# Kernel optimization log

Hardware: AMD Instinct MI355X
Metric: run time of the kernel (lower is better)

Reference implementation:

```python
import jax, jax.numpy as jnp
import numpy as np

D = 2048
H = 16
HD = D // H
FF = 4 * D
EPS = 1e-5


def layernorm(x, scale, shift):
    mean = jnp.mean(x, axis=-1, keepdims=True)
    var = jnp.mean((x - mean) ** 2, axis=-1, keepdims=True)  # unbiased=False
    return scale * (x - mean) / jnp.sqrt(var + EPS) + shift


def setup_inputs() -> dict:
    key = jax.random.key(0)
    ks = jax.random.split(key, 12)
    s = 0.02
    return {
        "x": jax.random.normal(ks[0], (2, 2048, D), dtype=jnp.float32),
        "ln1_scale": jnp.ones((D,), jnp.float32),
        "ln1_shift": jnp.zeros((D,), jnp.float32),
        "wq": jax.random.normal(ks[1], (D, D), jnp.float32) * s,
        "bq": jnp.zeros((D,), jnp.float32),
        "wk": jax.random.normal(ks[2], (D, D), jnp.float32) * s,
        "bk": jnp.zeros((D,), jnp.float32),
        "wv": jax.random.normal(ks[3], (D, D), jnp.float32) * s,
        "bv": jnp.zeros((D,), jnp.float32),
        "wo": jax.random.normal(ks[4], (D, D), jnp.float32) * s,
        "bo": jnp.zeros((D,), jnp.float32),
        "ln2_scale": jnp.ones((D,), jnp.float32),
        "ln2_shift": jnp.zeros((D,), jnp.float32),
        "w1": jax.random.normal(ks[5], (D, FF), jnp.float32) * s,
        "b1": jnp.zeros((FF,), jnp.float32),
        "w2": jax.random.normal(ks[6], (FF, D), jnp.float32) * s,
        "b2": jnp.zeros((D,), jnp.float32),
    }


def block(x, ln1_scale, ln1_shift, wq, bq, wk, bk, wv, bv, wo, bo,
          ln2_scale, ln2_shift, w1, b1, w2, b2):
    B, S, _ = x.shape
    h = layernorm(x, ln1_scale, ln1_shift)
    q = (h @ wq + bq).reshape(B, S, H, HD).transpose(0, 2, 1, 3)  # [B,H,S,hd]
    k = (h @ wk + bk).reshape(B, S, H, HD).transpose(0, 2, 1, 3)
    v = (h @ wv + bv).reshape(B, S, H, HD).transpose(0, 2, 1, 3)
    scores = jnp.einsum("bhqd,bhkd->bhqk", q, k) / jnp.sqrt(jnp.float32(HD))
    causal = jnp.tril(jnp.ones((S, S), dtype=bool))
    scores = jnp.where(causal[None, None], scores, -jnp.inf)
    attn = jax.nn.softmax(scores, axis=-1)
    ctx = jnp.einsum("bhqk,bhkd->bhqd", attn, v)
    ctx = ctx.transpose(0, 2, 1, 3).reshape(B, S, D)
    x = x + (ctx @ wo + bo)
    h2 = layernorm(x, ln2_scale, ln2_shift)
    ffn = jax.nn.gelu(h2 @ w1 + b1, approximate=False) @ w2 + b2
    return x + ffn


def reference(x, ln1_scale, ln1_shift, wq, bq, wk, bk, wv, bv, wo, bo,
              ln2_scale, ln2_shift, w1, b1, w2, b2):
    return block(x, ln1_scale, ln1_shift, wq, bq, wk, bk, wv, bv, wo, bo,
                 ln2_scale, ln2_shift, w1, b1, w2, b2)
```

## Files before the change

### kernel.cpp

```cpp
#include <hip/hip_runtime.h>
#include <hip/hip_bf16.h>
#include <math.h>

namespace {

constexpr int Dm  = 2048;
constexpr int FFm = 8192;
constexpr int SEQ = 2048;
constexpr int HDm = 128;
constexpr int MR  = 4096;
constexpr int QW  = 3 * Dm;

typedef __bf16 bf16_t;
typedef __bf16 bf16x8 __attribute__((ext_vector_type(8)));
typedef float  f32x4  __attribute__((ext_vector_type(4)));

typedef __attribute__((address_space(1))) const void as1_void;
typedef __attribute__((address_space(3))) void as3_void;

__device__ __forceinline__ void gload_lds16(const void* g, void* l) {
  __builtin_amdgcn_global_load_lds((as1_void*)g, (as3_void*)l, 16, 0, 0);
}

__global__ __launch_bounds__(256)
void ln_kernel(const float* __restrict__ x, const float* __restrict__ sc,
               const float* __restrict__ sh, bf16_t* __restrict__ out)
{
  const int row = blockIdx.x;
  const int tid = threadIdx.x;
  const float4* xr = (const float4*)(x + (size_t)row * Dm);
  float4 v0 = xr[tid*2], v1 = xr[tid*2+1];
  float s  = v0.x+v0.y+v0.z+v0.w + v1.x+v1.y+v1.z+v1.w;
  float s2 = v0.x*v0.x+v0.y*v0.y+v0.z*v0.z+v0.w*v0.w
           + v1.x*v1.x+v1.y*v1.y+v1.z*v1.z+v1.w*v1.w;
  #pragma unroll
  for (int off = 32; off; off >>= 1) { s += __shfl_xor(s, off); s2 += __shfl_xor(s2, off); }
  __shared__ float red[8];
  if ((tid & 63) == 0) { red[(tid>>6)*2] = s; red[(tid>>6)*2+1] = s2; }
  __syncthreads();
  s  = red[0]+red[2]+red[4]+red[6];
  s2 = red[1]+red[3]+red[5]+red[7];
  const float mean = s * (1.f/Dm);
  const float var  = fmaxf(s2 * (1.f/Dm) - mean*mean, 0.f);
  const float rstd = rsqrtf(var + 1e-5f);
  const float4* scp = (const float4*)sc;
  const float4* shp = (const float4*)sh;
  float4 sc0 = scp[tid*2], sc1 = scp[tid*2+1];
  float4 sh0 = shp[tid*2], sh1 = shp[tid*2+1];
  __attribute__((aligned(16))) bf16_t ob[8];
  ob[0] = (bf16_t)((v0.x-mean)*rstd*sc0.x + sh0.x);
  ob[1] = (bf16_t)((v0.y-mean)*rstd*sc0.y + sh0.y);
  ob[2] = (bf16_t)((v0.z-mean)*rstd*sc0.z + sh0.z);
  ob[3] = (bf16_t)((v0.w-mean)*rstd*sc0.w + sh0.w);
  ob[4] = (bf16_t)((v1.x-mean)*rstd*sc1.x + sh1.x);
  ob[5] = (bf16_t)((v1.y-mean)*rstd*sc1.y + sh1.y);
  ob[6] = (bf16_t)((v1.z-mean)*rstd*sc1.z + sh1.z);
  ob[7] = (bf16_t)((v1.w-mean)*rstd*sc1.w + sh1.w);
  *(uint4*)(out + (size_t)row*Dm + tid*8) = *(const uint4*)ob;
}

__global__ __launch_bounds__(256)
void wconv4(const float* __restrict__ wq, const float* __restrict__ wk,
            const float* __restrict__ wv, const float* __restrict__ wo,
            bf16_t* __restrict__ dst)
{
  const int z = blockIdx.z;
  const float* W = (z == 0) ? wq : (z == 1) ? wk : (z == 2) ? wv : wo;
  bf16_t* WT = dst + (size_t)z * Dm * Dm;
  __shared__ float tile[32][33];
  const int tx = threadIdx.x & 31, ty = threadIdx.x >> 5;
  const int nb = blockIdx.x * 32, kb = blockIdx.y * 32;
  #pragma unroll
  for (int p = 0; p < 4; ++p)
    tile[ty+8*p][tx] = W[(size_t)(kb+ty+8*p)*Dm + nb + tx];
  __syncthreads();
  #pragma unroll
  for (int p = 0; p < 4; ++p)
    WT[(size_t)(nb+ty+8*p)*Dm + kb + tx] = (bf16_t)tile[tx][ty+8*p];
}

__global__ __launch_bounds__(256)
void wconv_t(const float* __restrict__ W, bf16_t* __restrict__ WT, int K, int N)
{
  __shared__ float tile[32][33];
  const int tx = threadIdx.x & 31, ty = threadIdx.x >> 5;
  const int nb = blockIdx.x * 32, kb = blockIdx.y * 32;
  #pragma unroll
  for (int p = 0; p < 4; ++p)
    tile[ty+8*p][tx] = W[(size_t)(kb+ty+8*p)*N + nb + tx];
  __syncthreads();
  #pragma unroll
  for (int p = 0; p < 4; ++p)
    WT[(size_t)(nb+ty+8*p)*K + kb + tx] = (bf16_t)tile[tx][ty+8*p];
}

__global__ void bias_concat(const float* __restrict__ bq, const float* __restrict__ bk,
                            const float* __restrict__ bv, float* __restrict__ o)
{
  int i = blockIdx.x*256 + threadIdx.x;
  o[i] = bq[i]; o[Dm+i] = bk[i]; o[2*Dm+i] = bv[i];
}

__global__ __launch_bounds__(256)
void vtrans(const bf16_t* __restrict__ qkv, bf16_t* __restrict__ vT)
{
  __shared__ bf16_t tile[32][33];
  const int tx = threadIdx.x & 31, ty = threadIdx.x >> 5;
  const int s0 = blockIdx.x*32, d0 = blockIdx.y*32, bh = blockIdx.z;
  const int b = bh >> 4, h = bh & 15;
  const bf16_t* src = qkv + (size_t)(b*SEQ)*QW + 2*Dm + h*HDm;
  #pragma unroll
  for (int p = 0; p < 4; ++p)
    tile[ty+8*p][tx] = src[(size_t)(s0+ty+8*p)*QW + d0 + tx];
  __syncthreads();
  bf16_t* dst = vT + (size_t)bh*HDm*SEQ;
  #pragma unroll
  for (int p = 0; p < 4; ++p)
    dst[(size_t)(d0+ty+8*p)*SEQ + s0 + tx] = tile[tx][ty+8*p];
}

template<int MODE>
__global__ __launch_bounds__(512, 2)
void gemm8p(const bf16_t* __restrict__ A, const bf16_t* __restrict__ BT,
            const float* __restrict__ bias,
            void* __restrict__ Cout, void* __restrict__ Cout2,
            int Ndim, int Kslice, int Kstride, int gn)
{
  const int gm = (int)gridDim.x / gn;
  const int cm = gm >> 1, cn = gn >> 2;
  const int c = blockIdx.x & 7;
  const int idx = blockIdx.x >> 3;
  const int mi = idx / cn, ni = idx - mi*cn;
  const int m0 = ((c >> 2)*cm + mi) * 256;
  const int n0 = ((c & 3)*cn + ni) * 256;
  const int kOff = blockIdx.y * Kslice;
  const int tid = threadIdx.x;
  const int lane = tid & 63;
  const int w = tid >> 6;
  const int wr = w >> 2, wc = w & 3;
  const int lr = lane & 15, kg = lane >> 4;

  __shared__ __attribute__((aligned(16))) bf16_t lds[65536];

  f32x4 acc[8][4] = {};

  const int r1   = tid >> 3;
  const int blk1 = (tid & 7) ^ (r1 & 7);
  const size_t rowoff = (size_t)64 * Kstride;
  const bf16_t* pA0 = A  + (size_t)(m0 + r1)*Kstride       + kOff + blk1*8;
  const bf16_t* pA1 = A  + (size_t)(m0 + 128 + r1)*Kstride + kOff + blk1*8;
  const bf16_t* pB0 = BT + (size_t)(n0 + r1)*Kstride       + kOff + blk1*8;
  const bf16_t* pB1 = BT + (size_t)(n0 + 128 + r1)*Kstride + kOff + blk1*8;
  bf16_t* const d0 = lds + (size_t)tid*8;

#define STG(p, region) do { \
    gload_lds16((p), d0 + (region)*8192); \
    gload_lds16((p) + rowoff, d0 + (region)*8192 + 4096); \
    (p) += 64; } while (0)

  auto readA = [&](int buf, int mh, bf16x8* f) {
    const bf16_t* base = lds + (buf*4 + wr)*8192;
    #pragma unroll
    for (int ml = 0; ml < 4; ++ml)
      #pragma unroll
      for (int kk = 0; kk < 2; ++kk) {
        const int row = mh*64 + ml*16 + lr;
        f[ml*2+kk] = *(const bf16x8*)(base + row*64 + (((kk*4+kg) ^ (row&7))*8));
      }
  };
  auto readB = [&](int buf, int nh, bf16x8* f) {
    const bf16_t* base = lds + (buf*4 + 2 + (wc>>1))*8192;
    #pragma unroll
    for (int nl = 0; nl < 2; ++nl)
      #pragma unroll
      for (int kk = 0; kk < 2; ++kk) {
        const int row = (wc&1)*64 + nh*32 + nl*16 + lr;
        f[nl*2+kk] = *(const bf16x8*)(base + row*64 + (((kk*4+kg) ^ (row&7))*8));
      }
  };
  auto mfma16 = [&](int mh, int nh, const bf16x8* Af, const bf16x8* Bf) {
    __builtin_amdgcn_s_setprio(1);
    #pragma unroll
    for (int ml = 0; ml < 4; ++ml)
      #pragma unroll
      for (int nl = 0; nl < 2; ++nl)
        #pragma unroll
        for (int kk = 0; kk < 2; ++kk)
          acc[mh*4+ml][nh*2+nl] =
            __builtin_amdgcn_mfma_f32_16x16x32_bf16(Af[ml*2+kk], Bf[nl*2+kk],
                                                    acc[mh*4+ml][nh*2+nl], 0, 0, 0);
    __builtin_amdgcn_s_setprio(0);
  };

#define PHASE_MID() do { __builtin_amdgcn_s_barrier(); \
    asm volatile("s_waitcnt lgkmcnt(0)"); } while (0)
#define PHASE_END() __builtin_amdgcn_s_barrier()
#define KGUARD(more_) do { if (more_) asm volatile("s_waitcnt vmcnt(4)" ::: "memory"); \
    else asm volatile("s_waitcnt vmcnt(0)" ::: "memory"); \
    __builtin_amdgcn_s_barrier(); } while (0)

  STG(pA0, 0); STG(pA1, 1); STG(pB0, 2); STG(pB1, 3);
  STG(pA0, 4); STG(pA1, 5);
  asm volatile("s_waitcnt vmcnt(4)" ::: "memory");
  __builtin_amdgcn_s_barrier();

  const int NITER = Kslice >> 7;
  for (int j = 0; j < NITER; ++j) {
    const bool more = (j + 1 < NITER);
    bf16x8 Af0[8], Af1[8], Bf0[4], Bf1[4];

    readA(0,0,Af0); readB(0,0,Bf0);
    STG(pB0, 6);
    PHASE_MID(); mfma16(0,0,Af0,Bf0); PHASE_END();
    readA(0,1,Af1);
    STG(pB1, 7);
    PHASE_MID(); mfma16(1,0,Af1,Bf0); PHASE_END();
    readB(0,1,Bf1);
    if (more) STG(pA0, 0);
    PHASE_MID(); mfma16(1,1,Af1,Bf1); PHASE_END();
    if (more) STG(pA1, 1);
    PHASE_MID(); mfma16(0,1,Af0,Bf1);
    KGUARD(more);

    readA(1,0,Af0); readB(1,0,Bf0);
    if (more) STG(pB0, 2);
    PHASE_MID(); mfma16(0,0,Af0,Bf0); PHASE_END();
    readA(1,1,Af1);
    if (more) STG(pB1, 3);
    PHASE_MID(); mfma16(1,0,Af1,Bf0); PHASE_END();
    readB(1,1,Bf1);
    if (more) STG(pA0, 4);
    PHASE_MID(); mfma16(1,1,Af1,Bf1); PHASE_END();
    if (more) STG(pA1, 5);
    PHASE_MID(); mfma16(0,1,Af0,Bf1);
    KGUARD(more);
  }
#undef PHASE_MID
#undef PHASE_END
#undef KGUARD
#undef STG

  const int cr0 = m0 + wr*128 + kg*4;
  float* pout = nullptr;
  if constexpr (MODE == 3) pout = (float*)(blockIdx.y ? Cout2 : Cout);
  #pragma unroll
  for (int nf = 0; nf < 4; ++nf) {
    const int col = n0 + wc*64 + nf*16 + lr;
    float bv = 0.f;
    if constexpr (MODE != 3) bv = bias[col];
    #pragma unroll
    for (int mf = 0; mf < 8; ++mf) {
      const int rbase = cr0 + mf*16;
      #pragma unroll
      for (int jj = 0; jj < 4; ++jj) {
        float v = acc[mf][nf][jj] + bv;
        const size_t idx = (size_t)(rbase + jj)*Ndim + col;
        if constexpr (MODE == 1) v = 0.5f*v*(1.f + erff(v*0.70710678118f));
        if constexpr (MODE == 0 || MODE == 1) ((bf16_t*)Cout)[idx] = (bf16_t)v;
        else pout[idx] = v;
      }
    }
  }
}

__global__ __launch_bounds__(256)
void splitk_reduce(const float* __restrict__ p0, const float* __restrict__ p1,
                   const float* __restrict__ bias, const float* __restrict__ resid,
                   float* __restrict__ out, int Ndim)
{
  const size_t e = ((size_t)blockIdx.x*256 + threadIdx.x) * 4;
  float4 a = *(const float4*)(p0 + e);
  float4 b = *(const float4*)(p1 + e);
  float4 r = *(const float4*)(resid + e);
  float4 bv = *(const float4*)(bias + (int)(e & (size_t)(Ndim - 1)));
  float4 o;
  o.x = a.x + b.x + bv.x + r.x;
  o.y = a.y + b.y + bv.y + r.y;
  o.z = a.z + b.z + bv.z + r.z;
  o.w = a.w + b.w + bv.w + r.w;
  *(float4*)(out + e) = o;
}

__global__ __launch_bounds__(512, 2)
void flash_attn3(const bf16_t* __restrict__ qkv, const bf16_t* __restrict__ vT,
                 bf16_t* __restrict__ ctx)
{
  const int bid = blockIdx.x;
  const int bh  = (bid & 7) + 8 * ((bid >> 3) & 3);
  const int qi  = 7 - (bid >> 5);
  const int b = bh >> 4, h = bh & 15;
  const int Q0 = qi * 256;
  const int tid = threadIdx.x;
  const int lane = tid & 63;
  const int w = tid >> 6;
  const int lr = lane & 15, kg = lane >> 4;
  const int q0w = Q0 + w * 32;

  __shared__ __attribute__((aligned(16))) bf16_t Ks[64*128];
  __shared__ __attribute__((aligned(16))) bf16_t Vs[128*64];
  __shared__ __attribute__((aligned(16))) bf16_t Plds[8*2048];

  const bf16_t* kbase = qkv + (size_t)(b*SEQ)*QW + Dm + h*HDm;
  const bf16_t* vbase = vT + (size_t)bh*HDm*SEQ;

  bf16x8 qf[2][4];
  #pragma unroll
  for (int rt = 0; rt < 2; ++rt) {
    const bf16_t* qb = qkv + (size_t)(b*SEQ + q0w + rt*16 + lr)*QW + h*HDm;
    #pragma unroll
    for (int g = 0; g < 4; ++g)
      qf[rt][g] = *(const bf16x8*)(qb + g*32 + kg*8);
  }

  const float scl = 0.08838834764831845f * 1.44269504089f;
  float mrow[2][4], lsum[2][4];
  f32x4 oacc[2][8];
  #pragma unroll
  for (int rt = 0; rt < 2; ++rt) {
    #pragma unroll
    for (int j = 0; j < 4; ++j) { mrow[rt][j] = -INFINITY; lsum[rt][j] = 0.f; }
    #pragma unroll
    for (int dt = 0; dt < 8; ++dt) oacc[rt][dt] = (f32x4){0.f,0.f,0.f,0.f};
  }

  auto stage = [&](int k0) {
    #pragma unroll
    for (int i = 0; i < 2; ++i) {
      const int s = tid + i*512;
      const int row = s >> 4, sl = s & 15;
      gload_lds16(kbase + (size_t)(k0 + row)*QW + (sl ^ (row & 7))*8, Ks + s*8);
    }
    #pragma unroll
    for (int i = 0; i < 2; ++i) {
      const int s = tid + i*512;
      const int row = s >> 3, sl = s & 7;
      gload_lds16(vbase + (size_t)row*SEQ + k0 + (sl ^ (row & 7))*8, Vs + s*8);
    }
  };

  const int nsteps = (Q0 + 256) >> 6;
  stage(0);
  for (int t = 0; t < nsteps; ++t) {
    const int k0 = t * 64;
    __syncthreads();
    if (k0 < q0w + 32) {
      f32x4 sa[2][4];
      #pragma unroll
      for (int rt = 0; rt < 2; ++rt)
        #pragma unroll
        for (int ct = 0; ct < 4; ++ct) sa[rt][ct] = (f32x4){0.f,0.f,0.f,0.f};
      #pragma unroll
      for (int ct = 0; ct < 4; ++ct) {
        const int krow = ct*16 + lr;
        #pragma unroll
        for (int g = 0; g < 4; ++g) {
          bf16x8 kf = *(const bf16x8*)(Ks + krow*128 + ((4*g + kg) ^ (krow & 7))*8);
          sa[0][ct] = __builtin_amdgcn_mfma_f32_16x16x32_bf16(qf[0][g], kf, sa[0][ct], 0, 0, 0);
          sa[1][ct] = __builtin_amdgcn_mfma_f32_16x16x32_bf16(qf[1][g], kf, sa[1][ct], 0, 0, 0);
        }
      }
      #pragma unroll
      for (int rt = 0; rt < 2; ++rt)
        #pragma unroll
        for (int ct = 0; ct < 4; ++ct)
          #pragma unroll
          for (int j = 0; j < 4; ++j) sa[rt][ct][j] *= scl;
      if (k0 + 63 > q0w) {
        #pragma unroll
        for (int ct = 0; ct < 4; ++ct) {
          const int kidx = k0 + ct*16 + lr;
          #pragma unroll
          for (int rt = 0; rt < 2; ++rt)
            #pragma unroll
            for (int j = 0; j < 4; ++j) {
              const int qidx = q0w + rt*16 + kg*4 + j;
              if (kidx > qidx) sa[rt][ct][j] = -INFINITY;
            }
        }
      }
      #pragma unroll
      for (int rt = 0; rt < 2; ++rt) {
        #pragma unroll
        for (int j = 0; j < 4; ++j) {
          const int prow = kg*4 + j;
          float x0 = sa[rt][0][j], x1 = sa[rt][1][j], x2 = sa[rt][2][j], x3 = sa[rt][3][j];
          float v = fmaxf(fmaxf(x0, x1), fmaxf(x2, x3));
          v = fmaxf(v, __shfl_xor(v, 1));
          v = fmaxf(v, __shfl_xor(v, 2));
          v = fmaxf(v, __shfl_xor(v, 4));
          v = fmaxf(v, __shfl_xor(v, 8));
          const float mn = fmaxf(mrow[rt][j], v);
          const float alpha = exp2f(mrow[rt][j] - mn);
          mrow[rt][j] = mn;
          float p0 = exp2f(x0 - mn), p1 = exp2f(x1 - mn);
          float p2 = exp2f(x2 - mn), p3 = exp2f(x3 - mn);
          float ss = (p0 + p1) + (p2 + p3);
          ss += __shfl_xor(ss, 1);
          ss += __shfl_xor(ss, 2);
          ss += __shfl_xor(ss, 4);
          ss += __shfl_xor(ss, 8);
          lsum[rt][j] = lsum[rt][j]*alpha + ss;
          #pragma unroll
          for (int dt = 0; dt < 8; ++dt) oacc[rt][dt][j] *= alpha;
          const int base = w*2048 + rt*1024 + prow*64;
          const int sw = (prow & 7) << 3;
          Plds[(base + ( 0 + lr)) ^ sw] = (bf16_t)p0;
          Plds[(base + (16 + lr)) ^ sw] = (bf16_t)p1;
          Plds[(base + (32 + lr)) ^ sw] = (bf16_t)p2;
          Plds[(base + (48 + lr)) ^ sw] = (bf16_t)p3;
        }
      }
      bf16x8 pf[2][2];
      {
        const int sw = (lr & 7) << 3;
        #pragma unroll
        for (int rt = 0; rt < 2; ++rt) {
          pf[rt][0] = *(const bf16x8*)(Plds + ((w*2048 + rt*1024 + lr*64 +      kg*8) ^ sw));
          pf[rt][1] = *(const bf16x8*)(Plds + ((w*2048 + rt*1024 + lr*64 + 32 + kg*8) ^ sw));
        }
      }
      #pragma unroll
      for (int dt = 0; dt < 8; ++dt) {
        const int vrow = dt*16 + lr;
        #pragma unroll
        for (int kc = 0; kc < 2; ++kc) {
          bf16x8 vf = *(const bf16x8*)(Vs + vrow*64 + ((4*kc + kg) ^ (vrow & 7))*8);
          oacc[0][dt] = __builtin_amdgcn_mfma_f32_16x16x32_bf16(pf[0][kc], vf, oacc[0][dt], 0, 0, 0);
          oacc[1][dt] = __builtin_amdgcn_mfma_f32_16x16x32_bf16(pf[1][kc], vf, oacc[1][dt], 0, 0, 0);
        }
      }
    }
    __syncthreads();
    if (t + 1 < nsteps) stage((t + 1) * 64);
  }

  #pragma unroll
  for (int rt = 0; rt < 2; ++rt) {
    bf16_t* cb = ctx + (size_t)(b*SEQ + q0w + rt*16 + kg*4)*Dm + h*HDm;
    #pragma unroll
    for (int j = 0; j < 4; ++j) {
      const float inv = 1.f / lsum[rt][j];
      #pragma unroll
      for (int dt = 0; dt < 8; ++dt)
        cb[(size_t)j*Dm + dt*16 + lr] = (bf16_t)(oacc[rt][dt][j] * inv);
    }
  }
}

}

extern "C" void kernel_launch(void* const* d_in, const int* in_sizes, int n_in,
                              void* d_out, int out_size, void* d_ws, size_t ws_size,
                              hipStream_t stream)
{
  const float* x   = (const float*)d_in[0];
  const float* g1  = (const float*)d_in[1];
  const float* s1  = (const float*)d_in[2];
  const float* wq  = (const float*)d_in[3];
  const float* bq  = (const float*)d_in[4];
  const float* wk  = (const float*)d_in[5];
  const float* bk  = (const float*)d_in[6];
  const float* wv  = (const float*)d_in[7];
  const float* bv  = (const float*)d_in[8];
  const float* wo  = (const float*)d_in[9];
  const float* bo  = (const float*)d_in[10];
  const float* g2  = (const float*)d_in[11];
  const float* s2  = (const float*)d_in[12];
  const float* w1  = (const float*)d_in[13];
  const float* b1  = (const float*)d_in[14];
  const float* w2  = (const float*)d_in[15];
  const float* b2  = (const float*)d_in[16];
  float* out = (float*)d_out;

  char* p = (char*)d_ws;
  bf16_t* wqkvT = (bf16_t*)p;  p += (size_t)QW*Dm*2;
  bf16_t* woT   = (bf16_t*)p;  p += (size_t)Dm*Dm*2;
  bf16_t* w1T   = (bf16_t*)p;  p += (size_t)FFm*Dm*2;
  bf16_t* w2T   = (bf16_t*)p;  p += (size_t)Dm*FFm*2;
  float*  bqkv  = (float*)p;   p += (size_t)QW*4;
  bf16_t* hbuf  = (bf16_t*)p;  p += (size_t)MR*Dm*2;
  bf16_t* qkv   = (bf16_t*)p;  p += (size_t)MR*QW*2;
  bf16_t* vTb   = (bf16_t*)p;  p += (size_t)32*HDm*SEQ*2;
  bf16_t* ctx   = (bf16_t*)p;  p += (size_t)MR*Dm*2;
  float*  x1    = (float*)p;   p += (size_t)MR*Dm*4;
  bf16_t* ffn1  = qkv;
  float*  prj0  = (float*)qkv;
  float*  prj1  = (float*)qkv + (size_t)MR*Dm;
  float*  f2p0  = (float*)w1T;
  float*  f2p1  = (float*)wqkvT;

  wconv4<<<dim3(Dm/32, Dm/32, 4), 256, 0, stream>>>(wq, wk, wv, wo, wqkvT);
  wconv_t<<<dim3(FFm/32, Dm/32), 256, 0, stream>>>(w1, w1T, Dm, FFm);
  wconv_t<<<dim3(Dm/32, FFm/32), 256, 0, stream>>>(w2, w2T, FFm, Dm);
  bias_concat<<<dim3(Dm/256), 256, 0, stream>>>(bq, bk, bv, bqkv);

  ln_kernel<<<dim3(MR), 256, 0, stream>>>(x, g1, s1, hbuf);
  gemm8p<0><<<dim3((QW/256)*(MR/256), 1), 512, 0, stream>>>(
      hbuf, wqkvT, bqkv, qkv, nullptr, QW, Dm, Dm, QW/256);
  vtrans<<<dim3(SEQ/32, HDm/32, 32), 256, 0, stream>>>(qkv, vTb);
  flash_attn3<<<dim3(256), 512, 0, stream>>>(qkv, vTb, ctx);
  gemm8p<3><<<dim3((Dm/256)*(MR/256), 2), 512, 0, stream>>>(
      ctx, woT, nullptr, prj0, prj1, Dm, Dm/2, Dm, Dm/256);
  splitk_reduce<<<dim3(MR*Dm/1024), 256, 0, stream>>>(prj0, prj1, bo, x, x1, Dm);
  ln_kernel<<<dim3(MR), 256, 0, stream>>>(x1, g2, s2, hbuf);
  gemm8p<1><<<dim3((FFm/256)*(MR/256), 1), 512, 0, stream>>>(
      hbuf, w1T, b1, ffn1, nullptr, FFm, Dm, Dm, FFm/256);
  gemm8p<3><<<dim3((Dm/256)*(MR/256), 2), 512, 0, stream>>>(
      ffn1, w2T, nullptr, f2p0, f2p1, Dm, FFm/2, FFm, Dm/256);
  splitk_reduce<<<dim3(MR*Dm/1024), 256, 0, stream>>>(f2p0, f2p1, b2, x1, out, Dm);
}
```

Measured before the change: 725.8 us.

## Restructure GEMM main loop to 64-wide K steps with prefetched A fragments; stage epilogue through LDS

The GEMM main loop is rewritten from a 128-K double phase into a per-64-K-tile loop that keeps A fragments in registers and prefetches the next tile's A fragments during the current MFMAs. It also adjusts the vmcnt waits for the new load order. The bf16 output epilogue now writes results into swizzled LDS and then stores 16-byte coalesced rows to global memory, instead of scattered 2-byte stores. The changes aim to reduce LDS read stalls and uncoalesced store traffic, at the cost of more careful waitcnt bookkeeping and an extra LDS round trip in the epilogue.

```diff
diff --git a/kernel.cpp b/kernel.cpp
--- a/kernel.cpp
+++ b/kernel.cpp
@@ -154,8 +154,8 @@
   bf16_t* const d0 = lds + (size_t)tid*8;
 
 #define STG(p, region) do { \
-    gload_lds16((p), d0 + (region)*8192); \
-    gload_lds16((p) + rowoff, d0 + (region)*8192 + 4096); \
+    gload_lds16((p), d0 + (size_t)(region)*8192); \
+    gload_lds16((p) + rowoff, d0 + (size_t)(region)*8192 + 4096); \
     (p) += 64; } while (0)
 
   auto readA = [&](int buf, int mh, bf16x8* f) {
@@ -192,72 +192,94 @@
     __builtin_amdgcn_s_setprio(0);
   };
 
-#define PHASE_MID() do { __builtin_amdgcn_s_barrier(); \
-    asm volatile("s_waitcnt lgkmcnt(0)"); } while (0)
-#define PHASE_END() __builtin_amdgcn_s_barrier()
-#define KGUARD(more_) do { if (more_) asm volatile("s_waitcnt vmcnt(4)" ::: "memory"); \
-    else asm volatile("s_waitcnt vmcnt(0)" ::: "memory"); \
-    __builtin_amdgcn_s_barrier(); } while (0)
+  bf16x8 Af0[8], Af1[8], Bf0[4], Bf1[4];
 
   STG(pA0, 0); STG(pA1, 1); STG(pB0, 2); STG(pB1, 3);
   STG(pA0, 4); STG(pA1, 5);
   asm volatile("s_waitcnt vmcnt(4)" ::: "memory");
   __builtin_amdgcn_s_barrier();
-
-  const int NITER = Kslice >> 7;
-  for (int j = 0; j < NITER; ++j) {
-    const bool more = (j + 1 < NITER);
-    bf16x8 Af0[8], Af1[8], Bf0[4], Bf1[4];
-
-    readA(0,0,Af0); readB(0,0,Bf0);
-    STG(pB0, 6);
-    PHASE_MID(); mfma16(0,0,Af0,Bf0); PHASE_END();
-    readA(0,1,Af1);
-    STG(pB1, 7);
-    PHASE_MID(); mfma16(1,0,Af1,Bf0); PHASE_END();
-    readB(0,1,Bf1);
-    if (more) STG(pA0, 0);
-    PHASE_MID(); mfma16(1,1,Af1,Bf1); PHASE_END();
-    if (more) STG(pA1, 1);
-    PHASE_MID(); mfma16(0,1,Af0,Bf1);
-    KGUARD(more);
-
-    readA(1,0,Af0); readB(1,0,Bf0);
-    if (more) STG(pB0, 2);
-    PHASE_MID(); mfma16(0,0,Af0,Bf0); PHASE_END();
-    readA(1,1,Af1);
-    if (more) STG(pB1, 3);
-    PHASE_MID(); mfma16(1,0,Af1,Bf0); PHASE_END();
-    readB(1,1,Bf1);
-    if (more) STG(pA0, 4);
-    PHASE_MID(); mfma16(1,1,Af1,Bf1); PHASE_END();
-    if (more) STG(pA1, 5);
-    PHASE_MID(); mfma16(0,1,Af0,Bf1);
-    KGUARD(more);
+  readA(0, 0, Af0); readA(0, 1, Af1);
+
+  const int NT = Kslice >> 6;
+  for (int t = 0; t < NT; ++t) {
+    const int buf = t & 1, nbuf = buf ^ 1;
+    const bool s1 = (t + 1 < NT), s2 = (t + 2 < NT);
+
+    readB(buf, 0, Bf0);
+    if (s1) STG(pB0, nbuf*4 + 2);
+    __builtin_amdgcn_s_barrier();
+    asm volatile("s_waitcnt lgkmcnt(0)");
+    mfma16(0, 0, Af0, Bf0);
+    __builtin_amdgcn_s_barrier();
+
+    readB(buf, 1, Bf1);
+    if (s1) STG(pB1, nbuf*4 + 3);
+    __builtin_amdgcn_s_barrier();
+    asm volatile("s_waitcnt lgkmcnt(0)");
+    mfma16(0, 1, Af0, Bf1);
+    __builtin_amdgcn_s_barrier();
+
+    if (s2) STG(pA0, buf*4 + 0);
+    __builtin_amdgcn_s_barrier();
+    if (s2)      asm volatile("s_waitcnt vmcnt(6)" ::: "memory");
+    else if (s1) asm volatile("s_waitcnt vmcnt(4)" ::: "memory");
+    asm volatile("s_waitcnt lgkmcnt(0)");
+    if (s1) readA(nbuf, 0, Af0);
+    mfma16(1, 0, Af1, Bf0);
+    __builtin_amdgcn_s_barrier();
+
+    if (s2) STG(pA1, buf*4 + 1);
+    __builtin_amdgcn_s_barrier();
+    if (s2)      asm volatile("s_waitcnt vmcnt(8)" ::: "memory");
+    else if (s1) asm volatile("s_waitcnt vmcnt(4)" ::: "memory");
+    asm volatile("s_waitcnt lgkmcnt(0)");
+    mfma16(1, 1, Af1, Bf1);
+    if (s1) readA(nbuf, 1, Af1);
+    if (s2)      asm volatile("s_waitcnt vmcnt(4)" ::: "memory");
+    else if (s1) asm volatile("s_waitcnt vmcnt(0)" ::: "memory");
+    __builtin_amdgcn_s_barrier();
   }
-#undef PHASE_MID
-#undef PHASE_END
-#undef KGUARD
 #undef STG
 
   const int cr0 = m0 + wr*128 + kg*4;
-  float* pout = nullptr;
-  if constexpr (MODE == 3) pout = (float*)(blockIdx.y ? Cout2 : Cout);
-  #pragma unroll
-  for (int nf = 0; nf < 4; ++nf) {
-    const int col = n0 + wc*64 + nf*16 + lr;
-    float bv = 0.f;
-    if constexpr (MODE != 3) bv = bias[col];
-    #pragma unroll
-    for (int mf = 0; mf < 8; ++mf) {
-      const int rbase = cr0 + mf*16;
-      #pragma unroll
-      for (int jj = 0; jj < 4; ++jj) {
-        float v = acc[mf][nf][jj] + bv;
-        const size_t idx = (size_t)(rbase + jj)*Ndim + col;
-        if constexpr (MODE == 1) v = 0.5f*v*(1.f + erff(v*0.70710678118f));
-        if constexpr (MODE == 0 || MODE == 1) ((bf16_t*)Cout)[idx] = (bf16_t)v;
-        else pout[idx] = v;
+  if constexpr (MODE == 0 || MODE == 1) {
+    __syncthreads();
+    #pragma unroll
+    for (int nf = 0; nf < 4; ++nf) {
+      const int col = wc*64 + nf*16 + lr;
+      const float bv = bias[n0 + col];
+      #pragma unroll
+      for (int mf = 0; mf < 8; ++mf) {
+        #pragma unroll
+        for (int jj = 0; jj < 4; ++jj) {
+          float v = acc[mf][nf][jj] + bv;
+          if constexpr (MODE == 1) v = 0.5f*v*(1.f + erff(v*0.70710678118f));
+          const int row = wr*128 + mf*16 + kg*4 + jj;
+          const int adr = row*256 + (((col >> 3) ^ (row & 7)) << 3) + (col & 7);
+          lds[adr] = (bf16_t)v;
+        }
+      }
+    }
+    __syncthreads();
+    bf16_t* outp = (bf16_t*)Cout;
+    #pragma unroll
+    for (int i = 0; i < 16; ++i) {
+      const int s = tid + i*512;
+      const int row = s >> 5, ch = s & 31;
+      uint4 vv = *(const uint4*)(lds + row*256 + ((ch ^ (row & 7)) << 3));
+      *(uint4*)(outp + (size_t)(m0 + row)*Ndim + n0 + ch*8) = vv;
+    }
+  } else {
+    float* pout = (float*)(blockIdx.y ? Cout2 : Cout);
+    #pragma unroll
+    for (int nf = 0; nf < 4; ++nf) {
+      const int col = n0 + wc*64 + nf*16 + lr;
+      #pragma unroll
+      for (int mf = 0; mf < 8; ++mf) {
+        const int rbase = cr0 + mf*16;
+        #pragma unroll
+        for (int jj = 0; jj < 4; ++jj)
+          pout[(size_t)(rbase + jj)*Ndim + col] = acc[mf][nf][jj];
       }
     }
   }
```

Result: no change. 722.4 us (-0.5%).
